# Performance work log

Hardware: AMD Instinct MI355X
Metric: run time of the kernel (lower is better)

Reference implementation:

```python
import jax, jax.numpy as jnp
import numpy as np

B, S, H = 2, 2048, 2048
NH = 16
NOPE, ROPE, VDIM, RANK = 128, 64, 128, 512
QHD = NOPE + ROPE  # 192
MAX_POS, THETA = 4096, 50000.0
EPS = 1e-6


def rms_norm(x, w):
    var = jnp.mean(x.astype(jnp.float32) ** 2, axis=-1, keepdims=True)
    return (x * jax.lax.rsqrt(var + EPS)).astype(x.dtype) * w


def deinterleave(x):
    # view(..., d//2, 2).transpose(-1,-2).reshape(..., d): [x0,x2,...,x1,x3,...]
    return jnp.concatenate([x[..., ::2], x[..., 1::2]], axis=-1)


def rotate_half(x):
    x1, x2 = jnp.split(x, 2, axis=-1)
    return jnp.concatenate([-x2, x1], axis=-1)


def setup_inputs() -> dict:
    key = jax.random.key(0)
    ks = jax.random.split(key, 6)
    hidden_states = jax.random.normal(ks[0], (B, S, H), dtype=jnp.float32)
    attention_mask = jnp.broadcast_to(jnp.tril(jnp.ones((S, S), dtype=bool))[None, None], (B, 1, S, S))
    position_ids = jnp.broadcast_to(jnp.arange(S, dtype=jnp.int32)[None], (B, S))
    inv_freq = 1.0 / (THETA ** (jnp.arange(0, ROPE, 2, dtype=jnp.float32) / ROPE))
    freqs = jnp.arange(MAX_POS, dtype=jnp.float32)[:, None] * inv_freq[None, :]
    emb = jnp.concatenate([freqs, freqs], axis=-1)
    cos_cache, sin_cache = jnp.cos(emb), jnp.sin(emb)
    Wq = jax.random.normal(ks[1], (H, NH * QHD), dtype=jnp.float32) * 0.02
    Wkv_a = jax.random.normal(ks[2], (H, RANK + ROPE), dtype=jnp.float32) * 0.02
    kv_a_ln_w = jnp.ones((RANK,), dtype=jnp.float32)
    Wkv_b = jax.random.normal(ks[3], (NH, NOPE + VDIM, RANK), dtype=jnp.float32) * 0.02
    Wo = jax.random.normal(ks[4], (NH * VDIM, H), dtype=jnp.float32) * 0.02
    return {"hidden_states": hidden_states, "attention_mask": attention_mask, "position_ids": position_ids,
            "cos_cache": cos_cache, "sin_cache": sin_cache, "Wq": Wq, "Wkv_a": Wkv_a,
            "kv_a_ln_w": kv_a_ln_w, "Wkv_b": Wkv_b, "Wo": Wo}


def reference(hidden_states, attention_mask, position_ids, cos_cache, sin_cache, Wq, Wkv_a, kv_a_ln_w, Wkv_b, Wo):
    bsz, q_len, _ = hidden_states.shape
    scale = QHD ** (-0.5)
    # Q projection: [b,s,h*192] -> [b,h,s,192]
    q = (hidden_states @ Wq).reshape(bsz, q_len, NH, QHD).transpose(0, 2, 1, 3)
    q_nope, q_pe = q[..., :NOPE], q[..., NOPE:]
    # compressed KV + shared rope key: [b,s,576]
    ckv_full = hidden_states @ Wkv_a
    compressed_kv, k_pe = ckv_full[..., :RANK], ckv_full[..., RANK:]
    compressed_kv = rms_norm(compressed_kv, kv_a_ln_w)  # [b,s,512]
    # interleaved -> half layout, then standard RoPE
    q_pe = deinterleave(q_pe)                     # [b,h,s,64]
    k_pe = deinterleave(k_pe)                     # [b,s,64]
    cos = cos_cache[position_ids][:, None]        # [b,1,s,64]
    sin = sin_cache[position_ids][:, None]
    q_pe = q_pe * cos + rotate_half(q_pe) * sin
    k_pe = (k_pe[:, None] * cos + rotate_half(k_pe[:, None]) * sin)[:, 0]  # [b,s,64]
    # weight absorption
    q_absorb = Wkv_b[:, :NOPE]    # [h,128,512]
    out_absorb = Wkv_b[:, NOPE:]  # [h,128,512]
    q_nope_c = jnp.einsum('hdc,bhqd->bhqc', q_absorb, q_nope)  # [b,h,s,512]
    scores = (jnp.einsum('bhqd,bkd->bhqk', q_pe, k_pe)
              + jnp.einsum('bhqc,bkc->bhqk', q_nope_c, compressed_kv)) * scale
    scores = jnp.where(attention_mask, scores, jnp.float32(-1e9))
    probs = jax.nn.softmax(scores.astype(jnp.float32), axis=-1).astype(hidden_states.dtype)
    x = jnp.einsum('bhqk,bkc->bhqc', probs, compressed_kv)     # [b,h,s,512]
    attn = jnp.einsum('bhqc,hdc->bhqd', x, out_absorb)         # [b,h,s,128]
    attn = attn.transpose(0, 2, 1, 3).reshape(bsz, q_len, NH * VDIM)
    return attn @ Wo
```

## Files before the change

### kernel.cpp

```cpp
#include <hip/hip_runtime.h>
#include <math.h>

#define B_    2
#define S_    2048
#define H_    2048
#define NH_   16
#define NOPE_ 128
#define ROPE_ 64
#define VDIM_ 128
#define RANK_ 512
#define QHD_  192
#define DTOT_ 576

typedef short short8 __attribute__((ext_vector_type(8)));
typedef float f32x4 __attribute__((ext_vector_type(4)));

__device__ __forceinline__ unsigned short f2bf(float f) {
    unsigned u = __float_as_uint(f);
    u += 0x7fffu + ((u >> 16) & 1u);
    return (unsigned short)(u >> 16);
}
__device__ __forceinline__ float bf2f(unsigned short u) {
    return __uint_as_float((unsigned)u << 16);
}
__device__ __forceinline__ unsigned pack2bf(float a, float b) {
    return (unsigned)f2bf(a) | ((unsigned)f2bf(b) << 16);
}
__device__ __forceinline__ unsigned long long pack4bf(float a, float b, float c, float d) {
    return (unsigned long long)pack2bf(a, b) | ((unsigned long long)pack2bf(c, d) << 32);
}
union i4s8 { int4 i; short8 s; };

typedef __attribute__((address_space(3))) unsigned int lds_u32_t;
typedef __attribute__((address_space(1))) const unsigned int glob_u32_t;
__device__ __forceinline__ void async_copy16(const unsigned short* g, unsigned short* l) {
    __builtin_amdgcn_global_load_lds((glob_u32_t*)g, (lds_u32_t*)l, 16, 0, 0);
}

__global__ __launch_bounds__(256) void cast_bf16(const float* __restrict__ in,
                                                 unsigned short* __restrict__ out)
{
    const size_t i = ((size_t)blockIdx.x * 256 + threadIdx.x) * 4;
    float4 v = *(const float4*)(in + i);
    *(unsigned long long*)(out + i) = pack4bf(v.x, v.y, v.z, v.w);
}

__global__ __launch_bounds__(256) void transpose_w(const float* __restrict__ in,
                                                   unsigned short* __restrict__ out,
                                                   int Rr, int Cc,
                                                   size_t inBatch, size_t outBatch)
{
    __shared__ unsigned short tl[64][72];
    in  += (size_t)blockIdx.z * inBatch;
    out += (size_t)blockIdx.z * outBatch;
    const int t  = threadIdx.x;
    const int r0 = blockIdx.x * 64;
    const int c0 = blockIdx.y * 64;
    const int lr = t >> 4;
    const int lc = (t & 15) * 4;
#pragma unroll
    for (int r = 0; r < 4; ++r) {
        float4 v = *(const float4*)(in + (size_t)(r0 + lr*4 + r) * Cc + c0 + lc);
        tl[lr*4 + r][lc+0] = f2bf(v.x); tl[lr*4 + r][lc+1] = f2bf(v.y);
        tl[lr*4 + r][lc+2] = f2bf(v.z); tl[lr*4 + r][lc+3] = f2bf(v.w);
    }
    __syncthreads();
#pragma unroll
    for (int r = 0; r < 4; ++r) {
        ushort4 v;
        v.x = tl[lc+0][lr*4+r]; v.y = tl[lc+1][lr*4+r];
        v.z = tl[lc+2][lr*4+r]; v.w = tl[lc+3][lr*4+r];
        *(ushort4*)(out + (size_t)(c0 + lr*4 + r) * Rr + r0 + lc) = v;
    }
}

#define BGEMM_BODY(STORE_STMT)                                                     \
    __shared__ unsigned short Al[128*32];                                          \
    __shared__ unsigned short Bl[128*32];                                          \
    const int t = threadIdx.x;                                                     \
    const int wv = t >> 6;                                                         \
    const int lane = t & 63;                                                       \
    const int lq = lane & 15, quad = lane >> 4;                                    \
    const int m0 = blockIdx.y * 128, n0 = blockIdx.x * 128;                        \
    const int wrow = (wv >> 1) * 64, wcol = (wv & 1) * 64;                         \
    const int srow = lane >> 2;                                                    \
    const int scol = (lane & 3) * 8;                                               \
    f32x4 acc[4][4] = {};                                                          \
    for (int k0 = 0; k0 < K; k0 += 32) {                                           \
        _Pragma("unroll")                                                          \
        for (int pA = 0; pA < 2; ++pA) {                                           \
            const unsigned short* src =                                            \
                A + (size_t)(m0 + pA*64 + wv*16 + srow) * lda + k0 + scol;         \
            async_copy16(src, &Al[pA*2048 + wv*512]);                              \
        }                                                                          \
        _Pragma("unroll")                                                          \
        for (int pB = 0; pB < 2; ++pB) {                                           \
            int brow = n0 + pB*64 + wv*16 + srow;                                  \
            if (brow > N - 1) brow = N - 1;                                        \
            const unsigned short* src = B + (size_t)brow * K + k0 + scol;          \
            async_copy16(src, &Bl[pB*2048 + wv*512]);                              \
        }                                                                          \
        __syncthreads();                                                           \
        short8 af[4], bf[4];                                                       \
        _Pragma("unroll")                                                          \
        for (int i = 0; i < 4; ++i) {                                              \
            af[i] = *(const short8*)&Al[(wrow + i*16 + lq)*32 + quad*8];           \
            bf[i] = *(const short8*)&Bl[(wcol + i*16 + lq)*32 + quad*8];           \
        }                                                                          \
        _Pragma("unroll")                                                          \
        for (int mi = 0; mi < 4; ++mi)                                             \
            _Pragma("unroll")                                                      \
            for (int ni = 0; ni < 4; ++ni)                                         \
                acc[mi][ni] = __builtin_amdgcn_mfma_f32_16x16x32_bf16(             \
                    af[mi], bf[ni], acc[mi][ni], 0, 0, 0);                         \
        __syncthreads();                                                           \
    }                                                                              \
    _Pragma("unroll")                                                              \
    for (int mi = 0; mi < 4; ++mi)                                                 \
        _Pragma("unroll")                                                          \
        for (int ni = 0; ni < 4; ++ni) {                                           \
            int col = n0 + wcol + ni*16 + lq;                                      \
            if (col < N) {                                                         \
                _Pragma("unroll")                                                  \
                for (int r = 0; r < 4; ++r)                                        \
                    STORE_STMT;                                                    \
            }                                                                      \
        }

__global__ __launch_bounds__(256, 2) void bgemm2(const unsigned short* __restrict__ A,
                                                 int lda,
                                                 const unsigned short* __restrict__ B,
                                                 unsigned short* __restrict__ C,
                                                 int ldc, int K, int N, int qcmode)
{
    if (qcmode) {
        const int z = blockIdx.z;
        A += (size_t)(z >> 4) * S_ * (NH_*QHD_) + (z & 15) * QHD_;
        B += (size_t)(z & 15) * RANK_ * NOPE_;
        C += (size_t)z * S_ * DTOT_;
    }
    BGEMM_BODY(C[(size_t)(m0 + wrow + mi*16 + quad*4 + r) * ldc + col] = f2bf(acc[mi][ni][r]))
}

__global__ __launch_bounds__(256, 2) void bgemm2f(const unsigned short* __restrict__ A,
                                                  int lda,
                                                  const unsigned short* __restrict__ B,
                                                  float* __restrict__ C,
                                                  int ldc, int K, int N)
{
    BGEMM_BODY(C[(size_t)(m0 + wrow + mi*16 + quad*4 + r) * ldc + col] = acc[mi][ni][r])
}

__global__ __launch_bounds__(128) void postkv(const unsigned short* __restrict__ ckv_bf,
                                              const float* __restrict__ lnw,
                                              const int*   __restrict__ pos_ids,
                                              const float* __restrict__ cosc,
                                              const float* __restrict__ sinc,
                                              unsigned short* __restrict__ k_cat)
{
    const int row = blockIdx.x;
    const int t   = threadIdx.x;
    const unsigned short* src = ckv_bf + (size_t)row * DTOT_;
    __shared__ float red[128];

    ushort4 v = *(const ushort4*)(src + t * 4);
    float x0 = bf2f(v.x), x1 = bf2f(v.y), x2 = bf2f(v.z), x3 = bf2f(v.w);
    red[t] = x0*x0 + x1*x1 + x2*x2 + x3*x3;
    __syncthreads();
    for (int off = 64; off > 0; off >>= 1) {
        if (t < off) red[t] += red[t + off];
        __syncthreads();
    }
    const float rs = rsqrtf(red[0] / (float)RANK_ + 1e-6f);

    unsigned short* kc = k_cat + (size_t)row * DTOT_;
    *(unsigned long long*)(kc + t*4) =
        pack4bf(x0*rs*lnw[t*4+0], x1*rs*lnw[t*4+1], x2*rs*lnw[t*4+2], x3*rs*lnw[t*4+3]);

    if (t < 32) {
        const int pos = pos_ids[row];
        const float c  = cosc[pos * ROPE_ + t];
        const float sn = sinc[pos * ROPE_ + t];
        const float y0 = bf2f(src[RANK_ + 2*t]);
        const float y1 = bf2f(src[RANK_ + 2*t + 1]);
        kc[RANK_ + t]      = f2bf(y0*c - y1*sn);
        kc[RANK_ + 32 + t] = f2bf(y1*c + y0*sn);
    }
}

__global__ __launch_bounds__(512) void ropeq(const unsigned short* __restrict__ q_bf,
                                             const int*   __restrict__ pos_ids,
                                             const float* __restrict__ cosc,
                                             const float* __restrict__ sinc,
                                             unsigned short* __restrict__ q_cat)
{
    const int row = blockIdx.x;
    const int t   = threadIdx.x;
    const int h   = t >> 5;
    const int i   = t & 31;
    const int pos = pos_ids[row];
    const float c  = cosc[pos * ROPE_ + i];
    const float sn = sinc[pos * ROPE_ + i];
    const unsigned short* qrow = q_bf + (size_t)row * (NH_*QHD_) + h * QHD_ + NOPE_;
    const float x0 = bf2f(qrow[2*i]);
    const float x1 = bf2f(qrow[2*i + 1]);
    const int b = row >> 11, s = row & 2047;
    unsigned short* qc = q_cat + ((size_t)(b * NH_ + h) * S_ + s) * DTOT_ + RANK_;
    qc[i]      = f2bf(x0*c - x1*sn);
    qc[32 + i] = f2bf(x1*c + x0*sn);
}

__global__ __launch_bounds__(256) void transpose_v(const unsigned short* __restrict__ k_cat,
                                                   unsigned short* __restrict__ vt)
{
    __shared__ unsigned short tl[64][72];
    const int t  = threadIdx.x;
    const int k0 = blockIdx.x * 64;
    const int c0 = blockIdx.y * 64;
    const int b  = blockIdx.z;
    const int lr = t >> 4;
    const int lc = (t & 15) * 4;
#pragma unroll
    for (int r = 0; r < 4; ++r) {
        ushort4 v = *(const ushort4*)(k_cat + ((size_t)b * S_ + k0 + lr*4 + r) * DTOT_ + c0 + lc);
        tl[lr*4 + r][lc+0] = v.x; tl[lr*4 + r][lc+1] = v.y;
        tl[lr*4 + r][lc+2] = v.z; tl[lr*4 + r][lc+3] = v.w;
    }
    __syncthreads();
#pragma unroll
    for (int r = 0; r < 4; ++r) {
        ushort4 v;
        v.x = tl[lc+0][lr*4+r]; v.y = tl[lc+1][lr*4+r];
        v.z = tl[lc+2][lr*4+r]; v.w = tl[lc+3][lr*4+r];
        *(ushort4*)(vt + ((size_t)b * RANK_ + c0 + lr*4 + r) * S_ + k0 + lc) = v;
    }
}

__global__ __launch_bounds__(256) void wcast(const float* __restrict__ w,
                                             unsigned short* __restrict__ wbf)
{
    const size_t i = ((size_t)blockIdx.x * 256 + threadIdx.x) * 4;
    float4 v = *(const float4*)(w + i);
    *(unsigned long long*)(wbf + i) = pack4bf(v.x, v.y, v.z, v.w);
}

__device__ __forceinline__ short8 quad_transpose(unsigned d0, unsigned d1,
                                                 unsigned d2, unsigned d3,
                                                 int srcA, int srcB, bool lowquad)
{
    int e0 = __shfl((int)d0, srcA, 64);
    int e1 = __shfl((int)d1, srcA, 64);
    int e2 = __shfl((int)d2, srcA, 64);
    int e3 = __shfl((int)d3, srcA, 64);
    int f0 = __shfl((int)d0, srcB, 64);
    int f1 = __shfl((int)d1, srcB, 64);
    int f2 = __shfl((int)d2, srcB, 64);
    int f3 = __shfl((int)d3, srcB, 64);
    i4s8 u;
    u.i.x = lowquad ? e0 : e2;
    u.i.y = lowquad ? e1 : e3;
    u.i.z = lowquad ? f0 : f2;
    u.i.w = lowquad ? f1 : f3;
    return u.s;
}

__global__ __launch_bounds__(256, 2) void flash_attn4(
    const unsigned short* __restrict__ q_cat,
    const unsigned short* __restrict__ k_cat,
    const unsigned short* __restrict__ vt,
    const unsigned short* __restrict__ w2bf,
    unsigned short* __restrict__ attn_bf)
{
    __shared__ unsigned short sKa[32*512];
    __shared__ unsigned short sKb[32*64];
    __shared__ unsigned short sV[512*32];

    const int t    = threadIdx.x;
    const int wv   = t >> 6;
    const int lane = t & 63;
    const int lq   = lane & 15;
    const int quad = lane >> 4;
    const int h    = blockIdx.x;
    const int q0   = (31 - blockIdx.y) * 64;
    const int b    = blockIdx.z;
    const int srcA = lq + ((quad & 1) << 5);
    const int srcB = srcA + 16;
    const bool lowq = quad < 2;
    const int myq  = q0 + wv*16 + lq;

    const unsigned short* qrow =
        q_cat + (((size_t)(b*NH_ + h)) * S_ + q0 + wv*16 + lq) * DTOT_ + quad*8;
    short8 qf[18];
#pragma unroll
    for (int c = 0; c < 18; ++c) qf[c] = *(const short8*)(qrow + c*32);

    const unsigned short* kcb = k_cat + (size_t)b * S_ * DTOT_;
    const unsigned short* vtb = vt    + (size_t)b * RANK_ * S_;

    f32x4 o[32];
#pragma unroll
    for (int i = 0; i < 32; ++i) o[i] = (f32x4){0.f, 0.f, 0.f, 0.f};
    float m_i = -1e30f, l_i = 0.f;
    const float scale = 0.0721687836f;
    const int ntiles = (q0 >> 5) + 2;

    const int swz  = lq & 7;
    const int selA = (swz >> 2) * 32;
    const int selB = 32 - selA;
    const int kqo  = (quad ^ (swz & 3)) * 8;
    const unsigned short* kr0a = &sKa[lq*512 + kqo];
    const unsigned short* kr1a = &sKa[(16 + lq)*512 + kqo];
    const unsigned short* kr0b = &sKb[lq*64 + kqo];
    const unsigned short* kr1b = &sKb[(16 + lq)*64 + kqo];

    const int kq0 = wv*DTOT_ + (lane ^ wv)*8;
    const int kq1 = wv*DTOT_ + (lane ^ (wv + 4))*8;
    const int kob = (t >> 3)*DTOT_ + RANK_ + ((t & 7) ^ ((t >> 3) & 7))*8;

    const int vrow  = wv*16 + (lane >> 2);
    const int vgcol = (((lane & 3) ^ ((lane >> 2) & 3))) * 8;
    const int pvsw  = (quad ^ (lq & 3)) * 8;

#define ISSUE_K(TPTR)                                                          \
    _Pragma("unroll")                                                          \
    for (int p = 0; p < 8; ++p)                                                \
        async_copy16((TPTR) + (p*4)*DTOT_ + ((p & 1) ? kq1 : kq0),             \
                     &sKa[p*2048 + wv*512]);                                   \
    async_copy16((TPTR) + kob, &sKb[wv*512])

    const unsigned short* ktp = kcb;
    ISSUE_K(ktp);
    ktp += 32 * DTOT_;

    for (int tt = 0; tt < ntiles; ++tt) {
        const int k0 = tt << 5;
        __syncthreads();
        {
#pragma unroll
            for (int p = 0; p < 8; ++p) {
                const unsigned short* vsrc =
                    vtb + (size_t)(p*64 + vrow) * S_ + k0 + vgcol;
                async_copy16(vsrc, &sV[p*2048 + wv*512]);
            }
        }
        f32x4 s0a = {0.f,0.f,0.f,0.f}, s0b = {0.f,0.f,0.f,0.f};
        f32x4 s1a = {0.f,0.f,0.f,0.f}, s1b = {0.f,0.f,0.f,0.f};
#pragma unroll
        for (int c = 0; c < 16; c += 2) {
            short8 ka0 = *(const short8*)(kr0a + c*32 + selA);
            short8 kb0 = *(const short8*)(kr0a + c*32 + selB);
            short8 ka1 = *(const short8*)(kr1a + c*32 + selA);
            short8 kb1 = *(const short8*)(kr1a + c*32 + selB);
            s0a = __builtin_amdgcn_mfma_f32_16x16x32_bf16(ka0, qf[c],   s0a, 0, 0, 0);
            s1a = __builtin_amdgcn_mfma_f32_16x16x32_bf16(ka1, qf[c],   s1a, 0, 0, 0);
            s0b = __builtin_amdgcn_mfma_f32_16x16x32_bf16(kb0, qf[c+1], s0b, 0, 0, 0);
            s1b = __builtin_amdgcn_mfma_f32_16x16x32_bf16(kb1, qf[c+1], s1b, 0, 0, 0);
        }
        {
            short8 ka0 = *(const short8*)(kr0b + selA);
            short8 kb0 = *(const short8*)(kr0b + selB);
            short8 ka1 = *(const short8*)(kr1b + selA);
            short8 kb1 = *(const short8*)(kr1b + selB);
            s0a = __builtin_amdgcn_mfma_f32_16x16x32_bf16(ka0, qf[16], s0a, 0, 0, 0);
            s1a = __builtin_amdgcn_mfma_f32_16x16x32_bf16(ka1, qf[16], s1a, 0, 0, 0);
            s0b = __builtin_amdgcn_mfma_f32_16x16x32_bf16(kb0, qf[17], s0b, 0, 0, 0);
            s1b = __builtin_amdgcn_mfma_f32_16x16x32_bf16(kb1, qf[17], s1b, 0, 0, 0);
        }
        float sv[8];
#pragma unroll
        for (int r = 0; r < 4; ++r) {
            int kk0 = k0 + quad*4 + r;
            sv[r]     = (kk0      <= myq) ? (s0a[r] + s0b[r]) * scale : -1e30f;
            sv[r + 4] = (kk0 + 16 <= myq) ? (s1a[r] + s1b[r]) * scale : -1e30f;
        }
        float mx = sv[0];
#pragma unroll
        for (int i = 1; i < 8; ++i) mx = fmaxf(mx, sv[i]);
        mx = fmaxf(mx, __shfl_xor(mx, 16));
        mx = fmaxf(mx, __shfl_xor(mx, 32));
        if (!__all(mx <= m_i + 8.f)) {
            const float m_new = fmaxf(m_i, mx);
            const float alpha = __expf(m_i - m_new);
            m_i = m_new;
            l_i *= alpha;
#pragma unroll
            for (int i = 0; i < 32; ++i) {
                o[i][0]*=alpha; o[i][1]*=alpha; o[i][2]*=alpha; o[i][3]*=alpha;
            }
        }
        float p[8]; float ls = 0.f;
#pragma unroll
        for (int i = 0; i < 8; ++i) { p[i] = __expf(sv[i] - m_i); ls += p[i]; }
        ls += __shfl_xor(ls, 16);
        ls += __shfl_xor(ls, 32);
        l_i += ls;
        short8 pb = quad_transpose(pack2bf(p[0], p[1]), pack2bf(p[2], p[3]),
                                   pack2bf(p[4], p[5]), pack2bf(p[6], p[7]),
                                   srcA, srcB, lowq);
        __syncthreads();
        if (tt + 1 < ntiles) {
            ISSUE_K(ktp);
            ktp += 32 * DTOT_;
        }
#pragma unroll
        for (int ct = 0; ct < 32; ++ct) {
            short8 va = *(const short8*)&sV[(ct*16 + lq)*32 + pvsw];
            o[ct] = __builtin_amdgcn_mfma_f32_16x16x32_bf16(va, pb, o[ct], 0, 0, 0);
        }
    }

    const float inv = 1.0f / l_i;
    f32x4 acc[8];
#pragma unroll
    for (int i = 0; i < 8; ++i) acc[i] = (f32x4){0.f, 0.f, 0.f, 0.f};
    const unsigned short* wrow = w2bf + ((size_t)h*256 + NOPE_ + lq) * RANK_ + quad*8;
#pragma unroll
    for (int ch = 0; ch < 16; ++ch) {
        short8 xa = quad_transpose(
            pack2bf(o[2*ch][0]*inv,   o[2*ch][1]*inv),
            pack2bf(o[2*ch][2]*inv,   o[2*ch][3]*inv),
            pack2bf(o[2*ch+1][0]*inv, o[2*ch+1][1]*inv),
            pack2bf(o[2*ch+1][2]*inv, o[2*ch+1][3]*inv),
            srcA, srcB, lowq);
#pragma unroll
        for (int dt = 0; dt < 8; ++dt) {
            short8 wf = *(const short8*)(wrow + (size_t)dt*16*RANK_ + ch*32);
            acc[dt] = __builtin_amdgcn_mfma_f32_16x16x32_bf16(xa, wf, acc[dt], 0, 0, 0);
        }
    }
    unsigned short* orow =
        attn_bf + ((size_t)b * S_ + q0 + wv*16 + quad*4) * (NH_*VDIM_) + h*VDIM_ + lq;
#pragma unroll
    for (int dt = 0; dt < 8; ++dt)
#pragma unroll
        for (int r = 0; r < 4; ++r)
            orow[(size_t)r * (NH_*VDIM_) + dt*16] = f2bf(acc[dt][r]);
}

extern "C" void kernel_launch(void* const* d_in, const int* in_sizes, int n_in,
                              void* d_out, int out_size, void* d_ws, size_t ws_size,
                              hipStream_t stream)
{
    const float* hidden  = (const float*)d_in[0];
    const int*   pos_ids = (const int*)d_in[2];
    const float* cosc    = (const float*)d_in[3];
    const float* sinc    = (const float*)d_in[4];
    const float* Wq      = (const float*)d_in[5];
    const float* Wkv_a   = (const float*)d_in[6];
    const float* lnw     = (const float*)d_in[7];
    const float* Wkv_b   = (const float*)d_in[8];
    const float* Wo      = (const float*)d_in[9];
    float* out = (float*)d_out;

    const int M = B_ * S_;
    char* ws = (char*)d_ws;
    unsigned short* hidden_bf = (unsigned short*)ws;
    unsigned short* wqaT      = (unsigned short*)ws;
    unsigned short* attn_bf   = (unsigned short*)ws;
    unsigned short* q_bf      = (unsigned short*)(ws + 16777216);
    unsigned short* ckv_bf    = (unsigned short*)(ws + 41943040);
    unsigned short* vt        = ckv_bf;
    unsigned short* q_cat     = (unsigned short*)(ws + 46661632);
    unsigned short* k_cat     = (unsigned short*)(ws + 122159104);
    unsigned short* wT        = (unsigned short*)(ws + 126877696);
    unsigned short* w2bf      = (unsigned short*)(ws + 126877696 + 8388608);

    cast_bf16<<<8192, 256, 0, stream>>>(hidden, hidden_bf);
    transpose_w<<<dim3(32, 48, 1), 256, 0, stream>>>(Wq, wT, H_, NH_*QHD_, 0, 0);
    bgemm2<<<dim3(24, 32, 1), 256, 0, stream>>>(hidden_bf, H_, wT, q_bf, NH_*QHD_, H_, NH_*QHD_, 0);
    transpose_w<<<dim3(32, 9, 1), 256, 0, stream>>>(Wkv_a, wT, H_, DTOT_, 0, 0);
    bgemm2<<<dim3(5, 32, 1), 256, 0, stream>>>(hidden_bf, H_, wT, ckv_bf, DTOT_, H_, DTOT_, 0);
    postkv<<<M, 128, 0, stream>>>(ckv_bf, lnw, pos_ids, cosc, sinc, k_cat);
    ropeq<<<M, 512, 0, stream>>>(q_bf, pos_ids, cosc, sinc, q_cat);
    transpose_v<<<dim3(S_/64, RANK_/64, B_), 256, 0, stream>>>(k_cat, vt);
    wcast<<<(NH_*256*RANK_)/1024, 256, 0, stream>>>(Wkv_b, w2bf);
    transpose_w<<<dim3(2, 8, 16), 256, 0, stream>>>(Wkv_b, wqaT, NOPE_, RANK_,
                                                    (size_t)256*RANK_, (size_t)RANK_*NOPE_);
    bgemm2<<<dim3(4, 16, 32), 256, 0, stream>>>(q_bf, NH_*QHD_, wqaT, q_cat, DTOT_, NOPE_, RANK_, 1);
    flash_attn4<<<dim3(NH_, S_/64, B_), 256, 0, stream>>>(q_cat, k_cat, vt, w2bf, attn_bf);
    transpose_w<<<dim3(32, 32, 1), 256, 0, stream>>>(Wo, wT, H_, H_, 0, 0);
    bgemm2f<<<dim3(16, 32, 1), 256, 0, stream>>>(attn_bf, H_, wT, out, H_, H_, H_);
}
```

Before: 627.9 us.

## Pre-absorb output projection into per-head V so attention accumulates 128-dim outputs

```diff
diff --git a/kernel.cpp b/kernel.cpp
--- a/kernel.cpp
+++ b/kernel.cpp
@@ -97,7 +97,7 @@
         for (int pB = 0; pB < 2; ++pB) {                                           \
             int brow = n0 + pB*64 + wv*16 + srow;                                  \
             if (brow > N - 1) brow = N - 1;                                        \
-            const unsigned short* src = B + (size_t)brow * K + k0 + scol;          \
+            const unsigned short* src = B + (size_t)brow * ldb + k0 + scol;        \
             async_copy16(src, &Bl[pB*2048 + wv*512]);                              \
         }                                                                          \
         __syncthreads();                                                           \
@@ -130,14 +130,20 @@
 __global__ __launch_bounds__(256, 2) void bgemm2(const unsigned short* __restrict__ A,
                                                  int lda,
                                                  const unsigned short* __restrict__ B,
+                                                 int ldb,
                                                  unsigned short* __restrict__ C,
                                                  int ldc, int K, int N, int qcmode)
 {
-    if (qcmode) {
+    if (qcmode == 1) {
         const int z = blockIdx.z;
         A += (size_t)(z >> 4) * S_ * (NH_*QHD_) + (z & 15) * QHD_;
         B += (size_t)(z & 15) * RANK_ * NOPE_;
         C += (size_t)z * S_ * DTOT_;
+    } else if (qcmode == 2) {
+        const int z = blockIdx.z;
+        A += (size_t)(z & 15) * 256 * RANK_ + (size_t)NOPE_ * RANK_;
+        B += (size_t)(z >> 4) * S_ * DTOT_;
+        C += (size_t)z * VDIM_ * S_;
     }
     BGEMM_BODY(C[(size_t)(m0 + wrow + mi*16 + quad*4 + r) * ldc + col] = f2bf(acc[mi][ni][r]))
 }
@@ -145,6 +151,7 @@
 __global__ __launch_bounds__(256, 2) void bgemm2f(const unsigned short* __restrict__ A,
                                                   int lda,
                                                   const unsigned short* __restrict__ B,
+                                                  int ldb,
                                                   float* __restrict__ C,
                                                   int ldc, int K, int N)
 {
@@ -210,32 +217,6 @@
     qc[32 + i] = f2bf(x1*c + x0*sn);
 }
 
-__global__ __launch_bounds__(256) void transpose_v(const unsigned short* __restrict__ k_cat,
-                                                   unsigned short* __restrict__ vt)
-{
-    __shared__ unsigned short tl[64][72];
-    const int t  = threadIdx.x;
-    const int k0 = blockIdx.x * 64;
-    const int c0 = blockIdx.y * 64;
-    const int b  = blockIdx.z;
-    const int lr = t >> 4;
-    const int lc = (t & 15) * 4;
-#pragma unroll
-    for (int r = 0; r < 4; ++r) {
-        ushort4 v = *(const ushort4*)(k_cat + ((size_t)b * S_ + k0 + lr*4 + r) * DTOT_ + c0 + lc);
-        tl[lr*4 + r][lc+0] = v.x; tl[lr*4 + r][lc+1] = v.y;
-        tl[lr*4 + r][lc+2] = v.z; tl[lr*4 + r][lc+3] = v.w;
-    }
-    __syncthreads();
-#pragma unroll
-    for (int r = 0; r < 4; ++r) {
-        ushort4 v;
-        v.x = tl[lc+0][lr*4+r]; v.y = tl[lc+1][lr*4+r];
-        v.z = tl[lc+2][lr*4+r]; v.w = tl[lc+3][lr*4+r];
-        *(ushort4*)(vt + ((size_t)b * RANK_ + c0 + lr*4 + r) * S_ + k0 + lc) = v;
-    }
-}
-
 __global__ __launch_bounds__(256) void wcast(const float* __restrict__ w,
                                              unsigned short* __restrict__ wbf)
 {
@@ -267,13 +248,12 @@
 __global__ __launch_bounds__(256, 2) void flash_attn4(
     const unsigned short* __restrict__ q_cat,
     const unsigned short* __restrict__ k_cat,
-    const unsigned short* __restrict__ vt,
-    const unsigned short* __restrict__ w2bf,
+    const unsigned short* __restrict__ vwt,
     unsigned short* __restrict__ attn_bf)
 {
     __shared__ unsigned short sKa[32*512];
     __shared__ unsigned short sKb[32*64];
-    __shared__ unsigned short sV[512*32];
+    __shared__ unsigned short sVW[128*32];
 
     const int t    = threadIdx.x;
     const int wv   = t >> 6;
@@ -295,11 +275,11 @@
     for (int c = 0; c < 18; ++c) qf[c] = *(const short8*)(qrow + c*32);
 
     const unsigned short* kcb = k_cat + (size_t)b * S_ * DTOT_;
-    const unsigned short* vtb = vt    + (size_t)b * RANK_ * S_;
-
-    f32x4 o[32];
-#pragma unroll
-    for (int i = 0; i < 32; ++i) o[i] = (f32x4){0.f, 0.f, 0.f, 0.f};
+    const unsigned short* vtb = vwt + (size_t)(b*NH_ + h) * VDIM_ * S_;
+
+    f32x4 o[8];
+#pragma unroll
+    for (int i = 0; i < 8; ++i) o[i] = (f32x4){0.f, 0.f, 0.f, 0.f};
     float m_i = -1e30f, l_i = 0.f;
     const float scale = 0.0721687836f;
     const int ntiles = (q0 >> 5) + 2;
@@ -318,8 +298,8 @@
     const int kob = (t >> 3)*DTOT_ + RANK_ + ((t & 7) ^ ((t >> 3) & 7))*8;
 
     const int vrow  = wv*16 + (lane >> 2);
-    const int vgcol = (((lane & 3) ^ ((lane >> 2) & 3))) * 8;
-    const int pvsw  = (quad ^ (lq & 3)) * 8;
+    const int vgcol = (((lane & 3) ^ ((lane >> 3) & 3))) * 8;
+    const int pvsw  = (quad ^ ((lq >> 1) & 3)) * 8;
 
 #define ISSUE_K(TPTR)                                                          \
     _Pragma("unroll")                                                          \
@@ -337,10 +317,10 @@
         __syncthreads();
         {
 #pragma unroll
-            for (int p = 0; p < 8; ++p) {
+            for (int p = 0; p < 2; ++p) {
                 const unsigned short* vsrc =
                     vtb + (size_t)(p*64 + vrow) * S_ + k0 + vgcol;
-                async_copy16(vsrc, &sV[p*2048 + wv*512]);
+                async_copy16(vsrc, &sVW[p*2048 + wv*512]);
             }
         }
         f32x4 s0a = {0.f,0.f,0.f,0.f}, s0b = {0.f,0.f,0.f,0.f};
@@ -384,7 +364,7 @@
             m_i = m_new;
             l_i *= alpha;
 #pragma unroll
-            for (int i = 0; i < 32; ++i) {
+            for (int i = 0; i < 8; ++i) {
                 o[i][0]*=alpha; o[i][1]*=alpha; o[i][2]*=alpha; o[i][3]*=alpha;
             }
         }
@@ -403,38 +383,25 @@
             ktp += 32 * DTOT_;
         }
 #pragma unroll
-        for (int ct = 0; ct < 32; ++ct) {
-            short8 va = *(const short8*)&sV[(ct*16 + lq)*32 + pvsw];
-            o[ct] = __builtin_amdgcn_mfma_f32_16x16x32_bf16(va, pb, o[ct], 0, 0, 0);
+        for (int dt = 0; dt < 8; ++dt) {
+            short8 va = *(const short8*)&sVW[(dt*16 + lq)*32 + pvsw];
+            o[dt] = __builtin_amdgcn_mfma_f32_16x16x32_bf16(va, pb, o[dt], 0, 0, 0);
         }
     }
 
     const float inv = 1.0f / l_i;
-    f32x4 acc[8];
-#pragma unroll
-    for (int i = 0; i < 8; ++i) acc[i] = (f32x4){0.f, 0.f, 0.f, 0.f};
-    const unsigned short* wrow = w2bf + ((size_t)h*256 + NOPE_ + lq) * RANK_ + quad*8;
-#pragma unroll
-    for (int ch = 0; ch < 16; ++ch) {
+    unsigned short* orow =
+        attn_bf + ((size_t)b * S_ + q0 + wv*16 + lq) * (NH_*VDIM_) + h*VDIM_;
+#pragma unroll
+    for (int dt2 = 0; dt2 < 4; ++dt2) {
         short8 xa = quad_transpose(
-            pack2bf(o[2*ch][0]*inv,   o[2*ch][1]*inv),
-            pack2bf(o[2*ch][2]*inv,   o[2*ch][3]*inv),
-            pack2bf(o[2*ch+1][0]*inv, o[2*ch+1][1]*inv),
-            pack2bf(o[2*ch+1][2]*inv, o[2*ch+1][3]*inv),
+            pack2bf(o[2*dt2][0]*inv,   o[2*dt2][1]*inv),
+            pack2bf(o[2*dt2][2]*inv,   o[2*dt2][3]*inv),
+            pack2bf(o[2*dt2+1][0]*inv, o[2*dt2+1][1]*inv),
+            pack2bf(o[2*dt2+1][2]*inv, o[2*dt2+1][3]*inv),
             srcA, srcB, lowq);
-#pragma unroll
-        for (int dt = 0; dt < 8; ++dt) {
-            short8 wf = *(const short8*)(wrow + (size_t)dt*16*RANK_ + ch*32);
-            acc[dt] = __builtin_amdgcn_mfma_f32_16x16x32_bf16(xa, wf, acc[dt], 0, 0, 0);
-        }
-    }
-    unsigned short* orow =
-        attn_bf + ((size_t)b * S_ + q0 + wv*16 + quad*4) * (NH_*VDIM_) + h*VDIM_ + lq;
-#pragma unroll
-    for (int dt = 0; dt < 8; ++dt)
-#pragma unroll
-        for (int r = 0; r < 4; ++r)
-            orow[(size_t)r * (NH_*VDIM_) + dt*16] = f2bf(acc[dt][r]);
+        *(short8*)(orow + dt2*32 + quad*8) = xa;
+    }
 }
 
 extern "C" void kernel_launch(void* const* d_in, const int* in_sizes, int n_in,
@@ -455,11 +422,11 @@
     const int M = B_ * S_;
     char* ws = (char*)d_ws;
     unsigned short* hidden_bf = (unsigned short*)ws;
-    unsigned short* wqaT      = (unsigned short*)ws;
-    unsigned short* attn_bf   = (unsigned short*)ws;
+    unsigned short* vwT       = (unsigned short*)ws;
     unsigned short* q_bf      = (unsigned short*)(ws + 16777216);
+    unsigned short* attn_bf   = q_bf;
     unsigned short* ckv_bf    = (unsigned short*)(ws + 41943040);
-    unsigned short* vt        = ckv_bf;
+    unsigned short* wqaT      = ckv_bf;
     unsigned short* q_cat     = (unsigned short*)(ws + 46661632);
     unsigned short* k_cat     = (unsigned short*)(ws + 122159104);
     unsigned short* wT        = (unsigned short*)(ws + 126877696);
@@ -467,17 +434,17 @@
 
     cast_bf16<<<8192, 256, 0, stream>>>(hidden, hidden_bf);
     transpose_w<<<dim3(32, 48, 1), 256, 0, stream>>>(Wq, wT, H_, NH_*QHD_, 0, 0);
-    bgemm2<<<dim3(24, 32, 1), 256, 0, stream>>>(hidden_bf, H_, wT, q_bf, NH_*QHD_, H_, NH_*QHD_, 0);
+    bgemm2<<<dim3(24, 32, 1), 256, 0, stream>>>(hidden_bf, H_, wT, H_, q_bf, NH_*QHD_, H_, NH_*QHD_, 0);
     transpose_w<<<dim3(32, 9, 1), 256, 0, stream>>>(Wkv_a, wT, H_, DTOT_, 0, 0);
-    bgemm2<<<dim3(5, 32, 1), 256, 0, stream>>>(hidden_bf, H_, wT, ckv_bf, DTOT_, H_, DTOT_, 0);
+    bgemm2<<<dim3(5, 32, 1), 256, 0, stream>>>(hidden_bf, H_, wT, H_, ckv_bf, DTOT_, H_, DTOT_, 0);
     postkv<<<M, 128, 0, stream>>>(ckv_bf, lnw, pos_ids, cosc, sinc, k_cat);
     ropeq<<<M, 512, 0, stream>>>(q_bf, pos_ids, cosc, sinc, q_cat);
-    transpose_v<<<dim3(S_/64, RANK_/64, B_), 256, 0, stream>>>(k_cat, vt);
     wcast<<<(NH_*256*RANK_)/1024, 256, 0, stream>>>(Wkv_b, w2bf);
+    bgemm2<<<dim3(16, 1, 32), 256, 0, stream>>>(w2bf, RANK_, k_cat, DTOT_, vwT, S_, RANK_, S_, 2);
     transpose_w<<<dim3(2, 8, 16), 256, 0, stream>>>(Wkv_b, wqaT, NOPE_, RANK_,
                                                     (size_t)256*RANK_, (size_t)RANK_*NOPE_);
-    bgemm2<<<dim3(4, 16, 32), 256, 0, stream>>>(q_bf, NH_*QHD_, wqaT, q_cat, DTOT_, NOPE_, RANK_, 1);
-    flash_attn4<<<dim3(NH_, S_/64, B_), 256, 0, stream>>>(q_cat, k_cat, vt, w2bf, attn_bf);
+    bgemm2<<<dim3(4, 16, 32), 256, 0, stream>>>(q_bf, NH_*QHD_, wqaT, NOPE_, q_cat, DTOT_, NOPE_, RANK_, 1);
+    flash_attn4<<<dim3(NH_, S_/64, B_), 256, 0, stream>>>(q_cat, k_cat, vwT, attn_bf);
     transpose_w<<<dim3(32, 32, 1), 256, 0, stream>>>(Wo, wT, H_, H_, 0, 0);
-    bgemm2f<<<dim3(16, 32, 1), 256, 0, stream>>>(attn_bf, H_, wT, out, H_, H_, H_);
-}
+    bgemm2f<<<dim3(16, 32, 1), 256, 0, stream>>>(attn_bf, H_, wT, H_, out, H_, H_, H_);
+}
```

After: 523.6 us. 16.6% less time.
